# Performance work log

Measured on AMD Instinct MI355X. Metric: run time of the kernel, lower is better.

Reference implementation:

```python
import jax, jax.numpy as jnp
import numpy as np

N_NODES = 8192


def _gcn_norm(edge_index, num_nodes):
    # PyG GCNConv default: add self-loops, symmetric normalization.
    src, dst = edge_index[0], edge_index[1]
    loop = jnp.arange(num_nodes, dtype=src.dtype)
    src = jnp.concatenate([src, loop])
    dst = jnp.concatenate([dst, loop])
    deg = jax.ops.segment_sum(jnp.ones_like(dst, dtype=jnp.float32), dst,
                              num_segments=num_nodes)
    dis = jnp.where(deg > 0, jax.lax.rsqrt(jnp.maximum(deg, 1.0)), 0.0)
    norm = dis[src] * dis[dst]  # [E + N]
    return src, dst, norm


def _gcn_conv(x, W, b, src, dst, norm, num_nodes):
    h = x @ W                           # [N, F_out] dense GEMM
    msg = h[src] * norm[:, None]        # gather + scale, [E+N, F_out]
    out = jax.ops.segment_sum(msg, dst, num_segments=num_nodes)  # scatter-add
    return out + b


def setup_inputs() -> dict:
    key = jax.random.key(0)
    ks = jax.random.split(key, 8)
    N, E, F_in, H1, H2, F_out = N_NODES, 65536, 512, 4096, 1024, 10
    x = jax.random.normal(ks[0], (N, F_in), dtype=jnp.float32)
    edge_index = jax.random.randint(ks[1], (2, E), 0, N, dtype=jnp.int64)
    # Glorot-ish scaled weights
    W1 = jax.random.normal(ks[2], (F_in, H1), dtype=jnp.float32) * (1.0 / np.sqrt(F_in))
    b1 = jnp.zeros((H1,), dtype=jnp.float32)
    W2 = jax.random.normal(ks[3], (H1, H2), dtype=jnp.float32) * (1.0 / np.sqrt(H1))
    b2 = jnp.zeros((H2,), dtype=jnp.float32)
    W3 = jax.random.normal(ks[4], (H2, F_out), dtype=jnp.float32) * (1.0 / np.sqrt(H2))
    b3 = jnp.zeros((F_out,), dtype=jnp.float32)
    return {"x": x, "W1": W1, "b1": b1, "W2": W2, "b2": b2,
            "W3": W3, "b3": b3, "edge_index": edge_index}


def reference(x, W1, b1, W2, b2, W3, b3, edge_index):
    N = N_NODES
    src, dst, norm = _gcn_norm(edge_index, N)
    h = _gcn_conv(x.astype(jnp.float32), W1, b1, src, dst, norm, N)
    h = jax.nn.relu(h)  # dropout is identity in eval mode
    h = _gcn_conv(h, W2, b2, src, dst, norm, N)
    h = jax.nn.relu(h)
    h = _gcn_conv(h, W3, b3, src, dst, norm, N)
    return jax.nn.log_softmax(h, axis=1)
```

## Files before the change

kernel.cpp:

```cpp
#include <hip/hip_runtime.h>
#include <math.h>

#define N_NODES 8192
#define N_EDGES 65536
#define F_IN    512
#define HID1    4096
#define HID2    1024
#define F_OUT   10
#define H3_STRIDE 16
#define W3B_STRIDE 1032

typedef __bf16 bf16x8 __attribute__((ext_vector_type(8)));
typedef float floatx4 __attribute__((ext_vector_type(4)));
typedef float floatx16 __attribute__((ext_vector_type(16)));

static __device__ __forceinline__ unsigned short f2bf(float f) {
    union { float f; unsigned u; } v; v.f = f;
    unsigned r = v.u + 0x7fffu + ((v.u >> 16) & 1u);
    return (unsigned short)(r >> 16);
}
static __device__ __forceinline__ float bf2f(unsigned short u) {
    union { unsigned u; float f; } v; v.u = ((unsigned)u) << 16;
    return v.f;
}
static __device__ __forceinline__ void unpack8(uint4 r, float* f) {
    union { unsigned u; float v; } c;
    c.u = r.x << 16;          f[0] = c.v;
    c.u = r.x & 0xffff0000u;  f[1] = c.v;
    c.u = r.y << 16;          f[2] = c.v;
    c.u = r.y & 0xffff0000u;  f[3] = c.v;
    c.u = r.z << 16;          f[4] = c.v;
    c.u = r.z & 0xffff0000u;  f[5] = c.v;
    c.u = r.w << 16;          f[6] = c.v;
    c.u = r.w & 0xffff0000u;  f[7] = c.v;
}
static __device__ __forceinline__ uint4 pack8(const float* f) {
    uint4 o;
    o.x = (unsigned)f2bf(f[0]) | ((unsigned)f2bf(f[1]) << 16);
    o.y = (unsigned)f2bf(f[2]) | ((unsigned)f2bf(f[3]) << 16);
    o.z = (unsigned)f2bf(f[4]) | ((unsigned)f2bf(f[5]) << 16);
    o.w = (unsigned)f2bf(f[6]) | ((unsigned)f2bf(f[7]) << 16);
    return o;
}

__global__ __launch_bounds__(1024) void hist_scan_kernel(
        const int* __restrict__ ei, int* __restrict__ deg,
        int* __restrict__ row_ptr, int* __restrict__ cnt) {
    __shared__ int hist[N_NODES];
    __shared__ int sums[1024];
    int t = threadIdx.x;
#pragma unroll
    for (int i = 0; i < 8; i++) hist[t + i * 1024] = 0;
    __syncthreads();
    const int4* ei4 = (const int4*)(ei + N_EDGES);
#pragma unroll
    for (int i = 0; i < 16; i++) {
        int4 d4 = ei4[i * 1024 + t];
        atomicAdd(&hist[d4.x], 1);
        atomicAdd(&hist[d4.y], 1);
        atomicAdd(&hist[d4.z], 1);
        atomicAdd(&hist[d4.w], 1);
    }
    __syncthreads();
    int base = t * 8;
    int local[8], run = 0;
#pragma unroll
    for (int i = 0; i < 8; i++) {
        int dv = hist[base + i];
        deg[base + i] = dv;
        cnt[base + i] = 0;
        local[i] = run; run += dv;
    }
    sums[t] = run;
    __syncthreads();
    for (int off = 1; off < 1024; off <<= 1) {
        int val = (t >= off) ? sums[t - off] : 0;
        __syncthreads();
        sums[t] += val;
        __syncthreads();
    }
    int offset = (t == 0) ? 0 : sums[t - 1];
#pragma unroll
    for (int i = 0; i < 8; i++) row_ptr[base + i] = offset + local[i];
    if (t == 1023) row_ptr[N_NODES] = sums[1023];
}

static __device__ __forceinline__ void transpose_body(
        const float* __restrict__ W, unsigned short* __restrict__ Wt,
        int K, int N, int k0, int n0, int tid, float (*t)[33]) {
    int c = tid & 31, r8 = tid >> 5;
#pragma unroll
    for (int i = 0; i < 4; i++) {
        int r = r8 + i * 8;
        t[r][c] = W[(size_t)(k0 + r) * N + n0 + c];
    }
    __syncthreads();
#pragma unroll
    for (int i = 0; i < 4; i++) {
        int r = r8 + i * 8;
        Wt[(size_t)(n0 + r) * K + k0 + c] = f2bf(t[c][r]);
    }
}

__global__ __launch_bounds__(256) void megaprep_kernel(
        const int* __restrict__ ei, const int* __restrict__ deg,
        const int* __restrict__ row_ptr, int* __restrict__ cnt,
        int* __restrict__ csr_src, float* __restrict__ csr_w,
        const float* __restrict__ x, unsigned short* __restrict__ xb,
        const float* __restrict__ W1, unsigned short* __restrict__ W1t,
        const float* __restrict__ W2, unsigned short* __restrict__ W2t,
        const float* __restrict__ W3, unsigned short* __restrict__ w3b) {
    __shared__ float t[32][33];
    int b = blockIdx.x, tid = threadIdx.x;
    if (b < 256) {
        int e = b * 256 + tid;
        int s = ei[e];
        int d = ei[N_EDGES + e];
        int slot = row_ptr[d] + atomicAdd(&cnt[d], 1);
        csr_src[slot] = s;
        csr_w[slot] = rsqrtf((float)((deg[s] + 1) * (deg[d] + 1)));
    } else if (b < 4352) {
        int i = (b - 256) * 256 + tid;
        float4 a = ((const float4*)x)[i];
        ushort4 o;
        o.x = f2bf(a.x); o.y = f2bf(a.y); o.z = f2bf(a.z); o.w = f2bf(a.w);
        ((ushort4*)xb)[i] = o;
    } else if (b < 6400) {
        int bb = b - 4352;
        transpose_body(W1, W1t, F_IN, HID1, (bb >> 7) * 32, (bb & 127) * 32, tid, t);
    } else if (b < 10496) {
        int bb = b - 6400;
        transpose_body(W2, W2t, HID1, HID2, (bb >> 5) * 32, (bb & 31) * 32, tid, t);
    } else {
        for (int i = tid; i < HID2 * F_OUT; i += 256) {
            int k = i / F_OUT, c = i % F_OUT;
            w3b[c * W3B_STRIDE + k] = f2bf(W3[i]);
        }
    }
}

__global__ __launch_bounds__(256) void agg1_kernel(
        const unsigned short* __restrict__ xb, const int* __restrict__ row_ptr,
        const int* __restrict__ csr_src, const float* __restrict__ csr_w,
        const int* __restrict__ deg, unsigned short* __restrict__ out) {
    int v = blockIdx.x * 4 + (threadIdx.x >> 6);
    int t = threadIdx.x & 63;
    const uint4* xp = (const uint4*)xb;
    float sw = 1.0f / (float)(deg[v] + 1);
    float acc[8], tmp[8];
    unpack8(xp[(size_t)v * 64 + t], tmp);
#pragma unroll
    for (int j = 0; j < 8; j++) acc[j] = sw * tmp[j];
    int e = row_ptr[v], end = row_ptr[v + 1];
    for (; e + 4 <= end; e += 4) {
        int s0 = csr_src[e], s1 = csr_src[e + 1];
        int s2 = csr_src[e + 2], s3 = csr_src[e + 3];
        float w0 = csr_w[e], w1 = csr_w[e + 1];
        float w2 = csr_w[e + 2], w3 = csr_w[e + 3];
        float f0[8], f1[8], f2[8], f3[8];
        unpack8(xp[(size_t)s0 * 64 + t], f0);
        unpack8(xp[(size_t)s1 * 64 + t], f1);
        unpack8(xp[(size_t)s2 * 64 + t], f2);
        unpack8(xp[(size_t)s3 * 64 + t], f3);
#pragma unroll
        for (int j = 0; j < 8; j++)
            acc[j] += w0 * f0[j] + w1 * f1[j] + w2 * f2[j] + w3 * f3[j];
    }
    for (; e < end; e++) {
        int s = csr_src[e];
        float w = csr_w[e];
        float f0[8];
        unpack8(xp[(size_t)s * 64 + t], f0);
#pragma unroll
        for (int j = 0; j < 8; j++) acc[j] += w * f0[j];
    }
    ((uint4*)out)[(size_t)v * 64 + t] = pack8(acc);
}

__global__ __launch_bounds__(256) void agg2_gemm3_kernel(
        const unsigned short* __restrict__ h, const int* __restrict__ row_ptr,
        const int* __restrict__ csr_src, const float* __restrict__ csr_w,
        const int* __restrict__ deg, const float* __restrict__ b2,
        const unsigned short* __restrict__ w3b, float* __restrict__ H3) {
    __shared__ unsigned short w3s[F_OUT * W3B_STRIDE];
    __shared__ float red[4][F_OUT];
    int tid = threadIdx.x;
    for (int i = tid; i < F_OUT * W3B_STRIDE; i += 256) w3s[i] = w3b[i];
    __syncthreads();
    int half = tid >> 7;
    int t = tid & 127;
    int v = blockIdx.x * 2 + half;
    const uint4* hp = (const uint4*)h;
    float sw = 1.0f / (float)(deg[v] + 1);
    float acc[8], tmp[8];
    unpack8(hp[(size_t)v * 128 + t], tmp);
#pragma unroll
    for (int j = 0; j < 8; j++) acc[j] = sw * tmp[j];
    int e = row_ptr[v], end = row_ptr[v + 1];
    for (; e + 4 <= end; e += 4) {
        int s0 = csr_src[e], s1 = csr_src[e + 1];
        int s2 = csr_src[e + 2], s3 = csr_src[e + 3];
        float w0 = csr_w[e], w1 = csr_w[e + 1];
        float w2 = csr_w[e + 2], w3 = csr_w[e + 3];
        float f0[8], f1[8], f2[8], f3[8];
        unpack8(hp[(size_t)s0 * 128 + t], f0);
        unpack8(hp[(size_t)s1 * 128 + t], f1);
        unpack8(hp[(size_t)s2 * 128 + t], f2);
        unpack8(hp[(size_t)s3 * 128 + t], f3);
#pragma unroll
        for (int j = 0; j < 8; j++)
            acc[j] += w0 * f0[j] + w1 * f1[j] + w2 * f2[j] + w3 * f3[j];
    }
    for (; e < end; e++) {
        int s = csr_src[e];
        float w = csr_w[e];
        float f0[8];
        unpack8(hp[(size_t)s * 128 + t], f0);
#pragma unroll
        for (int j = 0; j < 8; j++) acc[j] += w * f0[j];
    }
    float4 b4a = ((const float4*)b2)[t * 2];
    float4 b4b = ((const float4*)b2)[t * 2 + 1];
    acc[0] = fmaxf(acc[0] + b4a.x, 0.0f); acc[1] = fmaxf(acc[1] + b4a.y, 0.0f);
    acc[2] = fmaxf(acc[2] + b4a.z, 0.0f); acc[3] = fmaxf(acc[3] + b4a.w, 0.0f);
    acc[4] = fmaxf(acc[4] + b4b.x, 0.0f); acc[5] = fmaxf(acc[5] + b4b.y, 0.0f);
    acc[6] = fmaxf(acc[6] + b4b.z, 0.0f); acc[7] = fmaxf(acc[7] + b4b.w, 0.0f);

    float partial[F_OUT];
#pragma unroll
    for (int c = 0; c < F_OUT; c++) {
        float wf[8];
        unpack8(*(const uint4*)&w3s[c * W3B_STRIDE + t * 8], wf);
        partial[c] = acc[0] * wf[0] + acc[1] * wf[1] + acc[2] * wf[2] + acc[3] * wf[3]
                   + acc[4] * wf[4] + acc[5] * wf[5] + acc[6] * wf[6] + acc[7] * wf[7];
    }
#pragma unroll
    for (int c = 0; c < F_OUT; c++) {
#pragma unroll
        for (int off = 32; off > 0; off >>= 1)
            partial[c] += __shfl_xor(partial[c], off, 64);
    }
    int wave = tid >> 6, lane = tid & 63;
    if (lane == 0) {
#pragma unroll
        for (int c = 0; c < F_OUT; c++) red[wave][c] = partial[c];
    }
    __syncthreads();
    if (tid < 2 * F_OUT) {
        int hh = tid / F_OUT, c = tid % F_OUT;
        H3[(size_t)(blockIdx.x * 2 + hh) * H3_STRIDE + c] =
            red[hh * 2][c] + red[hh * 2 + 1][c];
    }
}

#define P8_STAGE(mat_, kh_, dd_, base_, k0_) do {                              \
    unsigned short* L_ = lds + ((dd_) * 4 + (mat_) * 2 + (kh_)) * 8192;        \
    _Pragma("unroll")                                                          \
    for (int j = 0; j < 2; j++) {                                              \
        int slot = j * 512 + tid;                                              \
        int s4 = slot >> 4, cs = slot & 15;                                    \
        int csp = cs ^ (s4 & 3);                                               \
        int grow = s4 * 4 + (csp >> 2);                                        \
        int gcol = (csp & 3) * 8;                                              \
        __builtin_amdgcn_global_load_lds(                                      \
            (const __attribute__((address_space(1))) void*)((base_) + (size_t)grow * K + (k0_) + (kh_) * 32 + gcol), \
            (__attribute__((address_space(3))) void*)(&L_[slot * 8]), 16, 0, 0); \
    }                                                                          \
} while (0)

#define P8_OFF(R_, lc_) ((((R_) >> 2) * 128) + (((((R_) & 3) << 2) | (lc_)) ^ (((R_) >> 2) & 3)) * 8)

__global__ __launch_bounds__(512, 2) void gemm1_pipe8_kernel(
        const unsigned short* __restrict__ A,
        const unsigned short* __restrict__ Bt,
        const float* __restrict__ bias,
        unsigned short* __restrict__ C) {
    __shared__ unsigned short lds[65536];
    const int K = F_IN, N = HID1;
    int tid = threadIdx.x;
    int wave = tid >> 6, lane = tid & 63;
    int wm = wave >> 2, wn = wave & 3;
    int lrow = lane & 31, lhalf = lane >> 5;

    int b = blockIdx.x;
    int GN = HID1 >> 8;
    int ntile = (b >> 3) % GN;
    int mtile = ((b >> 3) / GN) * 8 + (b & 7);
    int m0 = mtile * 256, n0 = ntile * 256;

    const unsigned short* Abase = A + (size_t)m0 * K;
    const unsigned short* Bbase = Bt + (size_t)n0 * K;

    floatx16 acc[4][2] = {};
    const int NT = K >> 6;

    P8_STAGE(0, 0, 0, Abase, 0);
    P8_STAGE(1, 0, 0, Bbase, 0);
    P8_STAGE(0, 1, 0, Abase, 0);
    P8_STAGE(1, 1, 0, Bbase, 0);
    asm volatile("s_waitcnt vmcnt(4)" ::: "memory");
    __builtin_amdgcn_s_barrier();

    for (int t = 0; t < NT; t++) {
        int d = t & 1, dn = d ^ 1;
        int k1 = (t + 1) * 64;
#pragma unroll
        for (int kk = 0; kk < 4; kk++) {
            if (kk == 2) {
                if (t + 1 < NT)
                    asm volatile("s_waitcnt vmcnt(4)" ::: "memory");
                else
                    asm volatile("s_waitcnt vmcnt(0)" ::: "memory");
                __builtin_amdgcn_s_barrier();
            }
            int kh = kk >> 1;
            int lc0 = (kk & 1) * 2 + lhalf;
            const unsigned short* Ak = lds + (d * 4 + kh) * 8192;
            const unsigned short* Bk = lds + (d * 4 + 2 + kh) * 8192;
            bf16x8 af[4], bfr[2];
#pragma unroll
            for (int mt = 0; mt < 4; mt++) {
                int R = wm * 128 + mt * 32 + lrow;
                af[mt] = *(const bf16x8*)&Ak[P8_OFF(R, lc0)];
            }
#pragma unroll
            for (int nt = 0; nt < 2; nt++) {
                int R = wn * 64 + nt * 32 + lrow;
                bfr[nt] = *(const bf16x8*)&Bk[P8_OFF(R, lc0)];
            }
            if (t + 1 < NT) {
                if (kk == 0)      P8_STAGE(0, 0, dn, Abase, k1);
                else if (kk == 1) P8_STAGE(1, 0, dn, Bbase, k1);
                else if (kk == 2) P8_STAGE(0, 1, dn, Abase, k1);
                else              P8_STAGE(1, 1, dn, Bbase, k1);
            }
            __builtin_amdgcn_s_barrier();
            __builtin_amdgcn_s_setprio(1);
#pragma unroll
            for (int mt = 0; mt < 4; mt++)
#pragma unroll
                for (int nt = 0; nt < 2; nt++)
                    acc[mt][nt] = __builtin_amdgcn_mfma_f32_32x32x16_bf16(
                        af[mt], bfr[nt], acc[mt][nt], 0, 0, 0);
            __builtin_amdgcn_s_setprio(0);
            if (kk == 0 || kk == 2) __builtin_amdgcn_s_barrier();
        }
        asm volatile("s_waitcnt vmcnt(4)" ::: "memory");
        __builtin_amdgcn_s_barrier();
    }

#pragma unroll
    for (int mt = 0; mt < 4; mt++) {
#pragma unroll
        for (int nt = 0; nt < 2; nt++) {
            int col = n0 + wn * 64 + nt * 32 + lrow;
            float bv = bias[col];
#pragma unroll
            for (int reg = 0; reg < 16; reg++) {
                int row = m0 + wm * 128 + mt * 32 + (reg & 3) + 8 * (reg >> 2) + 4 * lhalf;
                float v = fmaxf(acc[mt][nt][reg] + bv, 0.0f);
                C[(size_t)row * N + col] = f2bf(v);
            }
        }
    }
}

template <bool OUT_BF16, bool BIAS, bool RELU>
__global__ __launch_bounds__(256) void gemm2_mfma_kernel(
        const unsigned short* __restrict__ A,
        const unsigned short* __restrict__ Bt,
        const float* __restrict__ bias,
        void* __restrict__ C,
        int M, int N, int K) {
    __shared__ unsigned short As[128 * 128];
    __shared__ unsigned short Bs[128 * 128];
    int tid = threadIdx.x;
    int wave = tid >> 6, lane = tid & 63;
    int wm = wave >> 1, wn = wave & 1;
    int GN = N >> 7;
    int b = blockIdx.x;
    int ntile = (b >> 3) % GN;
    int mtile = ((b >> 3) / GN) * 8 + (b & 7);
    int m0 = mtile * 128, n0 = ntile * 128;
    int lrow = lane & 31, lhalf = lane >> 5;

    floatx16 acc[2][2] = {};

    for (int k0 = 0; k0 < K; k0 += 128) {
#pragma unroll
        for (int j = 0; j < 8; j++) {
            int idx = j * 256 + tid;
            int r = idx >> 4;
            int kc = (idx & 15) ^ (r & 15);
            __builtin_amdgcn_global_load_lds(
                (const __attribute__((address_space(1))) void*)(A + (size_t)(m0 + r) * K + k0 + kc * 8),
                (__attribute__((address_space(3))) void*)(&As[idx * 8]), 16, 0, 0);
            __builtin_amdgcn_global_load_lds(
                (const __attribute__((address_space(1))) void*)(Bt + (size_t)(n0 + r) * K + k0 + kc * 8),
                (__attribute__((address_space(3))) void*)(&Bs[idx * 8]), 16, 0, 0);
        }
        __syncthreads();
#pragma unroll
        for (int kk = 0; kk < 8; kk++) {
            bf16x8 af[2], bfr[2];
            int c = kk * 2 + lhalf;
#pragma unroll
            for (int mt = 0; mt < 2; mt++) {
                int R = wm * 64 + mt * 32 + lrow;
                af[mt] = *(const bf16x8*)&As[(R * 16 + (c ^ (R & 15))) * 8];
            }
#pragma unroll
            for (int nt = 0; nt < 2; nt++) {
                int R = wn * 64 + nt * 32 + lrow;
                bfr[nt] = *(const bf16x8*)&Bs[(R * 16 + (c ^ (R & 15))) * 8];
            }
#pragma unroll
            for (int mt = 0; mt < 2; mt++)
#pragma unroll
                for (int nt = 0; nt < 2; nt++)
                    acc[mt][nt] = __builtin_amdgcn_mfma_f32_32x32x16_bf16(
                        af[mt], bfr[nt], acc[mt][nt], 0, 0, 0);
        }
        __syncthreads();
    }

#pragma unroll
    for (int mt = 0; mt < 2; mt++) {
#pragma unroll
        for (int nt = 0; nt < 2; nt++) {
            int col = n0 + wn * 64 + nt * 32 + lrow;
            float bv = BIAS ? bias[col] : 0.0f;
#pragma unroll
            for (int reg = 0; reg < 16; reg++) {
                int row = m0 + wm * 64 + mt * 32 + (reg & 3) + 8 * (reg >> 2) + 4 * lhalf;
                float v = acc[mt][nt][reg] + bv;
                if (RELU) v = fmaxf(v, 0.0f);
                if (OUT_BF16)
                    ((unsigned short*)C)[(size_t)row * N + col] = f2bf(v);
                else
                    ((float*)C)[(size_t)row * N + col] = v;
            }
        }
    }
}

__global__ void final_kernel(const float* __restrict__ h3, const int* __restrict__ row_ptr,
                             const int* __restrict__ csr_src, const float* __restrict__ csr_w,
                             const int* __restrict__ deg, const float* __restrict__ b3,
                             float* __restrict__ out) {
    int v = blockIdx.x * blockDim.x + threadIdx.x;
    if (v >= N_NODES) return;
    const float4* h4 = (const float4*)h3;
    float sw = 1.0f / (float)(deg[v] + 1);
    float a[12];
    *(float4*)&a[0] = h4[v * 4];
    *(float4*)&a[4] = h4[v * 4 + 1];
    *(float4*)&a[8] = h4[v * 4 + 2];
    float acc[F_OUT];
#pragma unroll
    for (int c = 0; c < F_OUT; c++) acc[c] = b3[c] + sw * a[c];
    int end = row_ptr[v + 1];
    for (int e = row_ptr[v]; e < end; e++) {
        int s = csr_src[e];
        float w = csr_w[e];
        float bsrc[12];
        *(float4*)&bsrc[0] = h4[s * 4];
        *(float4*)&bsrc[4] = h4[s * 4 + 1];
        *(float4*)&bsrc[8] = h4[s * 4 + 2];
#pragma unroll
        for (int c = 0; c < F_OUT; c++) acc[c] += w * bsrc[c];
    }
    float m = acc[0];
#pragma unroll
    for (int c = 1; c < F_OUT; c++) m = fmaxf(m, acc[c]);
    float ssum = 0.0f;
#pragma unroll
    for (int c = 0; c < F_OUT; c++) ssum += expf(acc[c] - m);
    float l = logf(ssum);
#pragma unroll
    for (int c = 0; c < F_OUT; c++) out[v * F_OUT + c] = acc[c] - m - l;
}

extern "C" void kernel_launch(void* const* d_in, const int* in_sizes, int n_in,
                              void* d_out, int out_size, void* d_ws, size_t ws_size,
                              hipStream_t stream) {
    const float* x  = (const float*)d_in[0];
    const float* W1 = (const float*)d_in[1];
    const float* b1 = (const float*)d_in[2];
    const float* W2 = (const float*)d_in[3];
    const float* b2 = (const float*)d_in[4];
    const float* W3 = (const float*)d_in[5];
    const float* b3 = (const float*)d_in[6];
    const int*   ei = (const int*)d_in[7];
    float* out = (float*)d_out;

    char* p = (char*)d_ws;
    int*   deg     = (int*)p;    p += N_NODES * 4;
    int*   cnt     = (int*)p;    p += N_NODES * 4;
    int*   row_ptr = (int*)p;    p += 33024;
    int*   csr_src = (int*)p;    p += N_EDGES * 4;
    float* csr_w   = (float*)p;  p += N_EDGES * 4;
    float* h3      = (float*)p;  p += N_NODES * H3_STRIDE * 4;
    unsigned short* w3b = (unsigned short*)p; p += (F_OUT * W3B_STRIDE * 2 + 255) / 256 * 256;
    unsigned short* xb    = (unsigned short*)p; p += (size_t)N_NODES * F_IN * 2;
    unsigned short* agg_x = (unsigned short*)p; p += (size_t)N_NODES * F_IN * 2;
    unsigned short* W1t   = (unsigned short*)p; p += (size_t)HID1 * F_IN * 2;
    unsigned short* W2t   = (unsigned short*)p; p += (size_t)HID2 * HID1 * 2;
    unsigned short* h1    = (unsigned short*)p; p += (size_t)N_NODES * HID1 * 2;
    unsigned short* h2pre = (unsigned short*)p; p += (size_t)N_NODES * HID2 * 2;

    hist_scan_kernel<<<1, 1024, 0, stream>>>(ei, deg, row_ptr, cnt);
    megaprep_kernel<<<10497, 256, 0, stream>>>(ei, deg, row_ptr, cnt, csr_src, csr_w,
                                               x, xb, W1, W1t, W2, W2t, W3, w3b);

    agg1_kernel<<<N_NODES / 4, 256, 0, stream>>>(xb, row_ptr, csr_src, csr_w, deg, agg_x);
    gemm1_pipe8_kernel<<<(N_NODES / 256) * (HID1 / 256) * 8 / 8, 512, 0, stream>>>(
        agg_x, W1t, b1, h1);

    gemm2_mfma_kernel<true, false, false><<<(HID2 / 128) * (N_NODES / 128), 256, 0, stream>>>(
        h1, W2t, nullptr, h2pre, N_NODES, HID2, HID1);

    agg2_gemm3_kernel<<<N_NODES / 2, 256, 0, stream>>>(h2pre, row_ptr, csr_src, csr_w,
                                                       deg, b2, w3b, h3);

    final_kernel<<<N_NODES / 256, 256, 0, stream>>>(h3, row_ptr, csr_src, csr_w, deg, b3, out);
}
```

Measured before the change: 284.0 us.

## Use pipelined 256x256 split-K GEMM for layer-2 with bf16 partial merge

Factors the double-buffered 256x256 MFMA main loop into a macro and reuses it for the second GEMM (8192x4096 @ 4096x1024). The K dimension is split in two so the launch has 256 blocks instead of 128 large tiles, filling more CUs. Each half writes bf16 partials (one into the now-unused xb buffer), and a new merge kernel adds them. The extra launch, extra memory traffic and double bf16 rounding of the partial sums are the tradeoff.

```diff
diff --git a/kernel.cpp b/kernel.cpp
--- a/kernel.cpp
+++ b/kernel.cpp
@@ -270,6 +270,61 @@
 
 #define P8_OFF(R_, lc_) ((((R_) >> 2) * 128) + (((((R_) & 3) << 2) | (lc_)) ^ (((R_) >> 2) & 3)) * 8)
 
+#define P8_MAIN_LOOP(NT_)                                                      \
+    P8_STAGE(0, 0, 0, Abase, 0);                                               \
+    P8_STAGE(1, 0, 0, Bbase, 0);                                               \
+    P8_STAGE(0, 1, 0, Abase, 0);                                               \
+    P8_STAGE(1, 1, 0, Bbase, 0);                                               \
+    asm volatile("s_waitcnt vmcnt(4)" ::: "memory");                           \
+    __builtin_amdgcn_s_barrier();                                              \
+    for (int t = 0; t < (NT_); t++) {                                          \
+        int d = t & 1, dn = d ^ 1;                                             \
+        int k1 = (t + 1) * 64;                                                 \
+        _Pragma("unroll")                                                      \
+        for (int kk = 0; kk < 4; kk++) {                                       \
+            if (kk == 2) {                                                     \
+                if (t + 1 < (NT_))                                             \
+                    asm volatile("s_waitcnt vmcnt(4)" ::: "memory");           \
+                else                                                           \
+                    asm volatile("s_waitcnt vmcnt(0)" ::: "memory");           \
+                __builtin_amdgcn_s_barrier();                                  \
+            }                                                                  \
+            int kh = kk >> 1;                                                  \
+            int lc0 = (kk & 1) * 2 + lhalf;                                    \
+            const unsigned short* Ak = lds + (d * 4 + kh) * 8192;              \
+            const unsigned short* Bk = lds + (d * 4 + 2 + kh) * 8192;          \
+            bf16x8 af[4], bfr[2];                                              \
+            _Pragma("unroll")                                                  \
+            for (int mt = 0; mt < 4; mt++) {                                   \
+                int R = wm * 128 + mt * 32 + lrow;                             \
+                af[mt] = *(const bf16x8*)&Ak[P8_OFF(R, lc0)];                  \
+            }                                                                  \
+            _Pragma("unroll")                                                  \
+            for (int nt = 0; nt < 2; nt++) {                                   \
+                int R = wn * 64 + nt * 32 + lrow;                              \
+                bfr[nt] = *(const bf16x8*)&Bk[P8_OFF(R, lc0)];                 \
+            }                                                                  \
+            if (t + 1 < (NT_)) {                                               \
+                if (kk == 0)      P8_STAGE(0, 0, dn, Abase, k1);               \
+                else if (kk == 1) P8_STAGE(1, 0, dn, Bbase, k1);               \
+                else if (kk == 2) P8_STAGE(0, 1, dn, Abase, k1);               \
+                else              P8_STAGE(1, 1, dn, Bbase, k1);               \
+            }                                                                  \
+            __builtin_amdgcn_s_barrier();                                      \
+            __builtin_amdgcn_s_setprio(1);                                     \
+            _Pragma("unroll")                                                  \
+            for (int mt = 0; mt < 4; mt++)                                     \
+                _Pragma("unroll")                                              \
+                for (int nt = 0; nt < 2; nt++)                                 \
+                    acc[mt][nt] = __builtin_amdgcn_mfma_f32_32x32x16_bf16(     \
+                        af[mt], bfr[nt], acc[mt][nt], 0, 0, 0);                \
+            __builtin_amdgcn_s_setprio(0);                                     \
+            if (kk == 0 || kk == 2) __builtin_amdgcn_s_barrier();              \
+        }                                                                      \
+        asm volatile("s_waitcnt vmcnt(4)" ::: "memory");                       \
+        __builtin_amdgcn_s_barrier();                                          \
+    }
+
 __global__ __launch_bounds__(512, 2) void gemm1_pipe8_kernel(
         const unsigned short* __restrict__ A,
         const unsigned short* __restrict__ Bt,
@@ -292,62 +347,7 @@
     const unsigned short* Bbase = Bt + (size_t)n0 * K;
 
     floatx16 acc[4][2] = {};
-    const int NT = K >> 6;
-
-    P8_STAGE(0, 0, 0, Abase, 0);
-    P8_STAGE(1, 0, 0, Bbase, 0);
-    P8_STAGE(0, 1, 0, Abase, 0);
-    P8_STAGE(1, 1, 0, Bbase, 0);
-    asm volatile("s_waitcnt vmcnt(4)" ::: "memory");
-    __builtin_amdgcn_s_barrier();
-
-    for (int t = 0; t < NT; t++) {
-        int d = t & 1, dn = d ^ 1;
-        int k1 = (t + 1) * 64;
-#pragma unroll
-        for (int kk = 0; kk < 4; kk++) {
-            if (kk == 2) {
-                if (t + 1 < NT)
-                    asm volatile("s_waitcnt vmcnt(4)" ::: "memory");
-                else
-                    asm volatile("s_waitcnt vmcnt(0)" ::: "memory");
-                __builtin_amdgcn_s_barrier();
-            }
-            int kh = kk >> 1;
-            int lc0 = (kk & 1) * 2 + lhalf;
-            const unsigned short* Ak = lds + (d * 4 + kh) * 8192;
-            const unsigned short* Bk = lds + (d * 4 + 2 + kh) * 8192;
-            bf16x8 af[4], bfr[2];
-#pragma unroll
-            for (int mt = 0; mt < 4; mt++) {
-                int R = wm * 128 + mt * 32 + lrow;
-                af[mt] = *(const bf16x8*)&Ak[P8_OFF(R, lc0)];
-            }
-#pragma unroll
-            for (int nt = 0; nt < 2; nt++) {
-                int R = wn * 64 + nt * 32 + lrow;
-                bfr[nt] = *(const bf16x8*)&Bk[P8_OFF(R, lc0)];
-            }
-            if (t + 1 < NT) {
-                if (kk == 0)      P8_STAGE(0, 0, dn, Abase, k1);
-                else if (kk == 1) P8_STAGE(1, 0, dn, Bbase, k1);
-                else if (kk == 2) P8_STAGE(0, 1, dn, Abase, k1);
-                else              P8_STAGE(1, 1, dn, Bbase, k1);
-            }
-            __builtin_amdgcn_s_barrier();
-            __builtin_amdgcn_s_setprio(1);
-#pragma unroll
-            for (int mt = 0; mt < 4; mt++)
-#pragma unroll
-                for (int nt = 0; nt < 2; nt++)
-                    acc[mt][nt] = __builtin_amdgcn_mfma_f32_32x32x16_bf16(
-                        af[mt], bfr[nt], acc[mt][nt], 0, 0, 0);
-            __builtin_amdgcn_s_setprio(0);
-            if (kk == 0 || kk == 2) __builtin_amdgcn_s_barrier();
-        }
-        asm volatile("s_waitcnt vmcnt(4)" ::: "memory");
-        __builtin_amdgcn_s_barrier();
-    }
+    P8_MAIN_LOOP(8)
 
 #pragma unroll
     for (int mt = 0; mt < 4; mt++) {
@@ -365,82 +365,63 @@
     }
 }
 
-template <bool OUT_BF16, bool BIAS, bool RELU>
-__global__ __launch_bounds__(256) void gemm2_mfma_kernel(
+__global__ __launch_bounds__(512, 2) void gemm2_pipe8_split_kernel(
         const unsigned short* __restrict__ A,
         const unsigned short* __restrict__ Bt,
-        const float* __restrict__ bias,
-        void* __restrict__ C,
-        int M, int N, int K) {
-    __shared__ unsigned short As[128 * 128];
-    __shared__ unsigned short Bs[128 * 128];
+        unsigned short* __restrict__ Ca,
+        unsigned short* __restrict__ Cb) {
+    __shared__ unsigned short lds[65536];
+    const int K = HID1;
+    const int N = HID2;
     int tid = threadIdx.x;
     int wave = tid >> 6, lane = tid & 63;
-    int wm = wave >> 1, wn = wave & 1;
-    int GN = N >> 7;
+    int wm = wave >> 2, wn = wave & 3;
+    int lrow = lane & 31, lhalf = lane >> 5;
+
     int b = blockIdx.x;
-    int ntile = (b >> 3) % GN;
-    int mtile = ((b >> 3) / GN) * 8 + (b & 7);
-    int m0 = mtile * 128, n0 = ntile * 128;
-    int lrow = lane & 31, lhalf = lane >> 5;
-
-    floatx16 acc[2][2] = {};
-
-    for (int k0 = 0; k0 < K; k0 += 128) {
-#pragma unroll
-        for (int j = 0; j < 8; j++) {
-            int idx = j * 256 + tid;
-            int r = idx >> 4;
-            int kc = (idx & 15) ^ (r & 15);
-            __builtin_amdgcn_global_load_lds(
-                (const __attribute__((address_space(1))) void*)(A + (size_t)(m0 + r) * K + k0 + kc * 8),
-                (__attribute__((address_space(3))) void*)(&As[idx * 8]), 16, 0, 0);
-            __builtin_amdgcn_global_load_lds(
-                (const __attribute__((address_space(1))) void*)(Bt + (size_t)(n0 + r) * K + k0 + kc * 8),
-                (__attribute__((address_space(3))) void*)(&Bs[idx * 8]), 16, 0, 0);
-        }
-        __syncthreads();
-#pragma unroll
-        for (int kk = 0; kk < 8; kk++) {
-            bf16x8 af[2], bfr[2];
-            int c = kk * 2 + lhalf;
-#pragma unroll
-            for (int mt = 0; mt < 2; mt++) {
-                int R = wm * 64 + mt * 32 + lrow;
-                af[mt] = *(const bf16x8*)&As[(R * 16 + (c ^ (R & 15))) * 8];
-            }
-#pragma unroll
-            for (int nt = 0; nt < 2; nt++) {
-                int R = wn * 64 + nt * 32 + lrow;
-                bfr[nt] = *(const bf16x8*)&Bs[(R * 16 + (c ^ (R & 15))) * 8];
-            }
-#pragma unroll
-            for (int mt = 0; mt < 2; mt++)
-#pragma unroll
-                for (int nt = 0; nt < 2; nt++)
-                    acc[mt][nt] = __builtin_amdgcn_mfma_f32_32x32x16_bf16(
-                        af[mt], bfr[nt], acc[mt][nt], 0, 0, 0);
-        }
-        __syncthreads();
-    }
-
-#pragma unroll
-    for (int mt = 0; mt < 2; mt++) {
+    int u = b >> 3;
+    int col = u & 7;
+    int mtile = (u >> 3) * 8 + (b & 7);
+    int ntile = col >> 1;
+    int ksp = col & 1;
+    int m0 = mtile * 256, n0 = ntile * 256;
+    int koff = ksp * (HID1 / 2);
+
+    const unsigned short* Abase = A + (size_t)m0 * K + koff;
+    const unsigned short* Bbase = Bt + (size_t)n0 * K + koff;
+    unsigned short* Cout = ksp ? Cb : Ca;
+
+    floatx16 acc[4][2] = {};
+    P8_MAIN_LOOP(32)
+
+#pragma unroll
+    for (int mt = 0; mt < 4; mt++) {
 #pragma unroll
         for (int nt = 0; nt < 2; nt++) {
-            int col = n0 + wn * 64 + nt * 32 + lrow;
-            float bv = BIAS ? bias[col] : 0.0f;
+            int colc = n0 + wn * 64 + nt * 32 + lrow;
 #pragma unroll
             for (int reg = 0; reg < 16; reg++) {
-                int row = m0 + wm * 64 + mt * 32 + (reg & 3) + 8 * (reg >> 2) + 4 * lhalf;
-                float v = acc[mt][nt][reg] + bv;
-                if (RELU) v = fmaxf(v, 0.0f);
-                if (OUT_BF16)
-                    ((unsigned short*)C)[(size_t)row * N + col] = f2bf(v);
-                else
-                    ((float*)C)[(size_t)row * N + col] = v;
+                int row = m0 + wm * 128 + mt * 32 + (reg & 3) + 8 * (reg >> 2) + 4 * lhalf;
+                Cout[(size_t)row * N + colc] = f2bf(acc[mt][nt][reg]);
             }
         }
+    }
+}
+
+__global__ __launch_bounds__(256) void merge_kernel(
+        const unsigned short* __restrict__ Ca, unsigned short* __restrict__ Cb) {
+    const uint4* a4 = (const uint4*)Ca;
+    uint4* b4 = (uint4*)Cb;
+    int base = blockIdx.x * 1024 + threadIdx.x;
+#pragma unroll
+    for (int j = 0; j < 4; j++) {
+        int i = base + j * 256;
+        float fa[8], fb[8];
+        unpack8(a4[i], fa);
+        unpack8(b4[i], fb);
+#pragma unroll
+        for (int k = 0; k < 8; k++) fa[k] += fb[k];
+        b4[i] = pack8(fa);
     }
 }
 
@@ -508,17 +489,18 @@
     unsigned short* W2t   = (unsigned short*)p; p += (size_t)HID2 * HID1 * 2;
     unsigned short* h1    = (unsigned short*)p; p += (size_t)N_NODES * HID1 * 2;
     unsigned short* h2pre = (unsigned short*)p; p += (size_t)N_NODES * HID2 * 2;
+    unsigned short* h2a = xb;
 
     hist_scan_kernel<<<1, 1024, 0, stream>>>(ei, deg, row_ptr, cnt);
     megaprep_kernel<<<10497, 256, 0, stream>>>(ei, deg, row_ptr, cnt, csr_src, csr_w,
                                                x, xb, W1, W1t, W2, W2t, W3, w3b);
 
     agg1_kernel<<<N_NODES / 4, 256, 0, stream>>>(xb, row_ptr, csr_src, csr_w, deg, agg_x);
-    gemm1_pipe8_kernel<<<(N_NODES / 256) * (HID1 / 256) * 8 / 8, 512, 0, stream>>>(
+    gemm1_pipe8_kernel<<<(N_NODES / 256) * (HID1 / 256), 512, 0, stream>>>(
         agg_x, W1t, b1, h1);
 
-    gemm2_mfma_kernel<true, false, false><<<(HID2 / 128) * (N_NODES / 128), 256, 0, stream>>>(
-        h1, W2t, nullptr, h2pre, N_NODES, HID2, HID1);
+    gemm2_pipe8_split_kernel<<<256, 512, 0, stream>>>(h1, W2t, h2a, h2pre);
+    merge_kernel<<<1024, 256, 0, stream>>>(h2a, h2pre);
 
     agg2_gemm3_kernel<<<N_NODES / 2, 256, 0, stream>>>(h2pre, row_ptr, csr_src, csr_w,
                                                        deg, b2, w3b, h3);
```

Result: faster. 274.6 us (-3.3%).
